# Kernel optimization log

Measured on AMD Instinct MI355X. Metric: run time of the kernel, lower is better.

Reference implementation:

```python
import jax, jax.numpy as jnp
import numpy as np

B, S, V, H, L, NH, DH, F, T = 256, 64, 21128, 768, 12, 12, 64, 3072, 11


def _layernorm(x, g, b):
    m = x.mean(-1, keepdims=True)
    v = ((x - m) ** 2).mean(-1, keepdims=True)
    return (x - m) / jnp.sqrt(v + 1e-12) * g + b


def setup_inputs():
    key = jax.random.key(0)
    ks = iter(jax.random.split(key, 24))
    std = 0.02
    w = lambda shape: jax.random.normal(next(ks), shape, jnp.float32) * std
    return {
        "input_ids": jax.random.randint(next(ks), (B, S), 0, V),
        "attention_mask": jnp.ones((B, S), jnp.int32),
        "label": jax.random.randint(next(ks), (B, S), 0, T),
        "word_emb": w((V, H)),
        "pos_emb": w((S, H)),
        "tok_emb": w((2, H)),
        "emb_ln_g": jnp.ones((H,), jnp.float32),
        "emb_ln_b": jnp.zeros((H,), jnp.float32),
        "Wqkv": w((L, H, 3 * H)),
        "bqkv": jnp.zeros((L, 3 * H), jnp.float32),
        "Wo": w((L, H, H)),
        "bo": jnp.zeros((L, H), jnp.float32),
        "ln1_g": jnp.ones((L, H), jnp.float32),
        "ln1_b": jnp.zeros((L, H), jnp.float32),
        "W1": w((L, H, F)),
        "b1": jnp.zeros((L, F), jnp.float32),
        "W2": w((L, F, H)),
        "b2": jnp.zeros((L, H), jnp.float32),
        "ln2_g": jnp.ones((L, H), jnp.float32),
        "ln2_b": jnp.zeros((L, H), jnp.float32),
        "fc_w": w((H, T)),
        "fc_b": jnp.zeros((T,), jnp.float32),
        "crf_start": w((T,)),
        "crf_end": w((T,)),
        "crf_trans": w((T, T)),
    }


def _encode(ids, mask, word_emb, pos_emb, tok_emb, eg, eb, layer_params):
    x = word_emb[ids] + pos_emb[None] + tok_emb[0][None, None]  # [B,S,H]
    x = _layernorm(x, eg, eb)
    bias = (1.0 - mask.astype(x.dtype))[:, None, None, :] * -1e9  # [B,1,1,S]

    def layer(x, p):
        Wqkv, bqkv, Wo, bo, g1, b1n, W1, b1, W2, b2, g2, b2n = p
        q, k, v = jnp.split(x @ Wqkv + bqkv, 3, axis=-1)
        sh = lambda t: t.reshape(B, S, NH, DH).transpose(0, 2, 1, 3)
        att = jax.nn.softmax(
            jnp.einsum("bhqd,bhkd->bhqk", sh(q), sh(k)) / jnp.sqrt(jnp.float32(DH)) + bias, -1
        )
        o = jnp.einsum("bhqk,bhkd->bhqd", att, sh(v)).transpose(0, 2, 1, 3).reshape(B, S, H)
        x = _layernorm(x + o @ Wo + bo, g1, b1n)
        h = jax.nn.gelu(x @ W1 + b1)
        x = _layernorm(x + h @ W2 + b2, g2, b2n)
        return x, None

    x, _ = jax.lax.scan(layer, x, layer_params)
    return x


def _crf_llh(em, tags, maskf, start, end, trans):
    # torchcrf log-likelihood, batch_first. em:[B,S,T] tags:[B,S] maskf:[B,S]
    bidx = jnp.arange(B)
    score = start[tags[:, 0]] + em[bidx, 0, tags[:, 0]]

    def num_step(s, xs):
        e_t, tp, tc, m = xs
        return s + (trans[tp, tc] + e_t[bidx, tc]) * m, None

    score, _ = jax.lax.scan(
        num_step, score,
        (em[:, 1:].transpose(1, 0, 2), tags[:, :-1].T, tags[:, 1:].T, maskf[:, 1:].T),
    )
    last_idx = maskf.sum(-1).astype(jnp.int32) - 1
    score = score + end[tags[bidx, last_idx]]

    alpha = start[None] + em[:, 0]  # [B,T]

    def den_step(a, xs):
        e_t, m = xs
        nxt = jax.scipy.special.logsumexp(a[:, :, None] + trans[None] + e_t[:, None, :], axis=1)
        return jnp.where(m[:, None] > 0, nxt, a), None

    alpha, _ = jax.lax.scan(den_step, alpha, (em[:, 1:].transpose(1, 0, 2), maskf[:, 1:].T))
    denom = jax.scipy.special.logsumexp(alpha + end[None], axis=1)
    return score - denom


def _viterbi(em, maskf, start, end, trans):
    bidx = jnp.arange(B)

    def step(s, xs):
        e_t, m = xs
        cand = s[:, :, None] + trans[None]  # [B,T_prev,T_cur]
        best_prev = jnp.argmax(cand, axis=1)  # [B,T]
        ns = jnp.max(cand, axis=1) + e_t
        return jnp.where(m[:, None] > 0, ns, s), best_prev

    score, hist = jax.lax.scan(
        step, start[None] + em[:, 0], (em[:, 1:].transpose(1, 0, 2), maskf[:, 1:].T)
    )  # hist: [S-1,B,T]
    last = jnp.argmax(score + end[None], axis=1)  # [B]

    def back(t, xs):
        h, m = xs
        nt = jnp.where(m > 0, h[bidx, t], t)
        return nt, nt

    _, prev_tags = jax.lax.scan(back, last, (hist, maskf[:, 1:].T), reverse=True)
    return jnp.concatenate([prev_tags.transpose(1, 0), last[:, None]], axis=1)  # [B,S]


def reference(input_ids, attention_mask, label, word_emb, pos_emb, tok_emb, emb_ln_g, emb_ln_b,
              Wqkv, bqkv, Wo, bo, ln1_g, ln1_b, W1, b1, W2, b2, ln2_g, ln2_b,
              fc_w, fc_b, crf_start, crf_end, crf_trans):
    lp = (Wqkv, bqkv, Wo, bo, ln1_g, ln1_b, W1, b1, W2, b2, ln2_g, ln2_b)
    x = _encode(input_ids, attention_mask, word_emb, pos_emb, tok_emb, emb_ln_g, emb_ln_b, lp)
    logits = x @ fc_w + fc_b  # [B,S,T]
    maskf = attention_mask.astype(jnp.float32)
    loss = -jnp.mean(_crf_llh(logits, label, maskf, crf_start, crf_end, crf_trans))
    pred = _viterbi(logits, maskf, crf_start, crf_end, crf_trans)
    return pred, loss
```

## Files before the change

kernel.cpp:

```cpp
#include <hip/hip_runtime.h>
#include <hip/hip_bf16.h>
#include <math.h>

namespace {

constexpr int B = 256, S = 64, H = 768, L = 12, NH = 12, F = 3072, T = 11;
constexpr int BS = B * S;
constexpr int RC = 8192;
constexpr int NCH = BS / RC;

typedef __attribute__((ext_vector_type(8))) short short8;
typedef __attribute__((ext_vector_type(4))) float f32x4;

__device__ __forceinline__ float gelu_tanh(float v) {
  float u = 0.7978845608028654f * (v + 0.044715f * v * v * v);
  u = fminf(fmaxf(u, -10.f), 10.f);
  float t = __expf(2.f * u);
  return 0.5f * v * (1.0f + (t - 1.f) / (t + 1.f));
}

__device__ __forceinline__ ushort f2bf(float v) {
  union { float f; unsigned u; } c; c.f = v;
  unsigned r = (c.u + 0x7fffu + ((c.u >> 16) & 1u)) >> 16;
  return (ushort)r;
}
__device__ __forceinline__ float bf2f(ushort u) {
  union { unsigned u; float f; } c; c.u = ((unsigned)u) << 16;
  return c.f;
}
__device__ __forceinline__ void split2(float v, ushort& hi, ushort& lo) {
  hi = f2bf(v);
  lo = f2bf(v - bf2f(hi));
}
__device__ __forceinline__ float join2(ushort hi, ushort lo) {
  return bf2f(hi) + bf2f(lo);
}
__device__ __forceinline__ int pcol(int c) { return ((c >> 5) << 6) + (c & 31); }

#define GLOAD_LDS16(gptr, ldsptr)                                                        \
  __builtin_amdgcn_global_load_lds((const __attribute__((address_space(1))) void*)(gptr), \
                                   (__attribute__((address_space(3))) void*)(ldsptr), 16, 0, 0)

template <int MODE>
__global__ __launch_bounds__(256, 2) void gemm_mfma(const ushort* __restrict__ A,
                                                    const ushort* __restrict__ Bw,
                                                    const float* __restrict__ bias,
                                                    float* __restrict__ outF,
                                                    ushort* __restrict__ outU,
                                                    int lda2, int ldb2, int ldc2,
                                                    int ldcF, int zStrideF, int ktiles) {
  __shared__ ushort sA[2][128 * 64];
  __shared__ ushort sB[2][128 * 64];
  const int tid = threadIdx.x;
  const int w = tid >> 6;
  const int lane = tid & 63;
  const int wm = w >> 1;
  const int wn = w & 1;

  const int gx = gridDim.x, gy = gridDim.y;
  const int flat = ((int)blockIdx.z * gy + blockIdx.y) * gx + blockIdx.x;
  const int q8 = (gx * gy * (int)gridDim.z) >> 3;
  const int swz = (flat & 7) * q8 + (flat >> 3);
  const int bx = swz % gx;
  const int by = (swz / gx) % gy;
  const int bz = swz / (gx * gy);
  const int bm = by * 128;
  const int bn = bx * 128;
  const int k0 = bz * ktiles * 64;

  const int srow = lane >> 3;
  const int sblk = (lane & 7) ^ srow;
  const ushort* Ab = A + (size_t)(bm + w * 32 + srow) * lda2 + k0 + sblk * 8;
  const ushort* Bb = Bw + (size_t)(bn + w * 32 + srow) * ldb2 + k0 + sblk * 8;

#define STAGE(buf, tk)                                                            \
  do {                                                                            \
    _Pragma("unroll") for (int i_ = 0; i_ < 4; ++i_) {                            \
      GLOAD_LDS16(Ab + (size_t)(tk) * 64 + (size_t)(i_ * 8) * lda2,               \
                  &sA[buf][(w * 32 + i_ * 8) * 64]);                              \
      GLOAD_LDS16(Bb + (size_t)(tk) * 64 + (size_t)(i_ * 8) * ldb2,               \
                  &sB[buf][(w * 32 + i_ * 8) * 64]);                              \
    }                                                                             \
  } while (0)

  const int fr = lane & 15;
  const int s7 = fr & 7;
  const int jb = lane >> 4;
  const int hOff = (jb ^ s7) << 3;
  const int lOff = ((4 + jb) ^ s7) << 3;

  f32x4 acc[4][4] = {};
  const int NT = ktiles;

  STAGE(0, 0);
  asm volatile("s_waitcnt vmcnt(0)" ::: "memory");
  __builtin_amdgcn_s_barrier();

  for (int t = 0; t < NT; ++t) {
    const int cur = t & 1;
    if (t + 1 < NT) STAGE(cur ^ 1, t + 1);

    short8 ah[4], al[4];
#pragma unroll
    for (int mi = 0; mi < 4; ++mi) {
      const ushort* baseA = &sA[cur][(wm * 64 + mi * 16 + fr) * 64];
      ah[mi] = *(const short8*)(baseA + hOff);
      al[mi] = *(const short8*)(baseA + lOff);
    }
#pragma unroll
    for (int ni = 0; ni < 4; ++ni) {
      const ushort* baseB = &sB[cur][(wn * 64 + ni * 16 + fr) * 64];
      short8 bh = *(const short8*)(baseB + hOff);
      short8 bl = *(const short8*)(baseB + lOff);
      __builtin_amdgcn_s_setprio(1);
#pragma unroll
      for (int mi = 0; mi < 4; ++mi) {
        acc[mi][ni] = __builtin_amdgcn_mfma_f32_16x16x32_bf16(ah[mi], bh, acc[mi][ni], 0, 0, 0);
        acc[mi][ni] = __builtin_amdgcn_mfma_f32_16x16x32_bf16(ah[mi], bl, acc[mi][ni], 0, 0, 0);
        acc[mi][ni] = __builtin_amdgcn_mfma_f32_16x16x32_bf16(al[mi], bh, acc[mi][ni], 0, 0, 0);
      }
      __builtin_amdgcn_s_setprio(0);
      if (ni == 3) asm volatile("s_waitcnt vmcnt(0)" ::: "memory");
      __builtin_amdgcn_s_barrier();
    }
  }
#undef STAGE

  const int erow = jb << 2;
#pragma unroll
  for (int ni = 0; ni < 4; ++ni) {
    const int col = bn + wn * 64 + ni * 16 + fr;
    const float bv = (MODE == 3) ? 0.f : bias[col];
    const int cb = pcol(col);
#pragma unroll
    for (int mi = 0; mi < 4; ++mi) {
#pragma unroll
      for (int e = 0; e < 4; ++e) {
        const int row = bm + wm * 64 + mi * 16 + erow + e;
        float v = acc[mi][ni][e] + bv;
        if (MODE == 1 || MODE == 2) {
          if (MODE == 1) v = gelu_tanh(v);
          ushort hi, lo;
          split2(v, hi, lo);
          outU[(size_t)row * ldc2 + cb] = hi;
          outU[(size_t)row * ldc2 + cb + 32] = lo;
        } else {
          outF[(size_t)bz * zStrideF + (size_t)row * ldcF + col] = v;
        }
      }
    }
  }
}

__global__ __launch_bounds__(256) void convert_w_t(const float* __restrict__ W,
                                                   ushort* __restrict__ WI, int K, int N) {
  __shared__ float tile[32][33];
  const int kb = blockIdx.y * 32, nb = blockIdx.x * 32;
  const int tr = threadIdx.x >> 5;
  const int tc = threadIdx.x & 31;
#pragma unroll
  for (int p = 0; p < 4; ++p) {
    int r = tr + p * 8;
    tile[r][tc] = W[(size_t)(kb + r) * N + nb + tc];
  }
  __syncthreads();
  const int kblk = kb >> 5;
#pragma unroll
  for (int p = 0; p < 4; ++p) {
    int n = tr + p * 8;
    float v = tile[tc][n];
    ushort hi, lo;
    split2(v, hi, lo);
    size_t o = (size_t)(nb + n) * (2 * K) + (size_t)kblk * 64 + tc;
    WI[o] = hi;
    WI[o + 32] = lo;
  }
}

__global__ __launch_bounds__(256) void attn_kernel(ushort* __restrict__ qkv,
                                                   const int* __restrict__ mask) {
  __shared__ float smem[64 * 64 + 64 * 66 + 64 * 64];
  float (*Qs)[64] = (float (*)[64])smem;
  float (*KsT)[66] = (float (*)[66])(smem + 64 * 64);
  float (*Vs)[64] = (float (*)[64])(smem + 64 * 64 + 64 * 66);
  float (*Ps)[65] = (float (*)[65])smem;

  const int bl = blockIdx.x / NH;
  const int hh = blockIdx.x % NH;
  const int tid = threadIdx.x;
  const int lane = tid & 63;
  const int w = tid >> 6;

  for (int i = 0; i < 16; ++i) {
    int idx = tid + i * 256;
    int r = idx >> 6, d = idx & 63;
    size_t rowb = (size_t)(bl * 64 + r) * 4608;
    int off = hh * 128 + pcol(d);
    Qs[r][d] = join2(qkv[rowb + off], qkv[rowb + off + 32]);
    KsT[d][r] = join2(qkv[rowb + 1536 + off], qkv[rowb + 1536 + off + 32]);
    Vs[r][d] = join2(qkv[rowb + 3072 + off], qkv[rowb + 3072 + off + 32]);
  }
  __syncthreads();

  float sc[16];
#pragma unroll
  for (int i = 0; i < 16; ++i) sc[i] = 0.f;
  for (int d = 0; d < 64; ++d) {
    float kv = KsT[d][lane];
#pragma unroll
    for (int i = 0; i < 16; ++i) sc[i] += Qs[w + 4 * i][d] * kv;
  }
  __syncthreads();
  float biask = (1.0f - (float)mask[bl * S + lane]) * -1e9f;
#pragma unroll
  for (int i = 0; i < 16; ++i) Ps[w + 4 * i][lane] = sc[i] * 0.125f + biask;
  __syncthreads();

  if (tid < 64) {
    int qr = tid;
    float mx = -1e30f;
    for (int k = 0; k < 64; ++k) mx = fmaxf(mx, Ps[qr][k]);
    float sum = 0.f;
    for (int k = 0; k < 64; ++k) {
      float e = expf(Ps[qr][k] - mx);
      Ps[qr][k] = e;
      sum += e;
    }
    float inv = 1.0f / sum;
    for (int k = 0; k < 64; ++k) Ps[qr][k] *= inv;
  }
  __syncthreads();

  float o[16];
#pragma unroll
  for (int i = 0; i < 16; ++i) o[i] = 0.f;
  for (int k = 0; k < 64; ++k) {
    float vv = Vs[k][lane];
#pragma unroll
    for (int i = 0; i < 16; ++i) o[i] += Ps[w + 4 * i][k] * vv;
  }
  const int ooff = hh * 128 + pcol(lane);
#pragma unroll
  for (int i = 0; i < 16; ++i) {
    int qr = w + 4 * i;
    size_t rowb = (size_t)(bl * 64 + qr) * 4608;
    ushort hi, lo;
    split2(o[i], hi, lo);
    qkv[rowb + ooff] = hi;
    qkv[rowb + ooff + 32] = lo;
  }
}

__global__ __launch_bounds__(256) void embed_ln_kernel(const int* __restrict__ ids,
                                                       const float* __restrict__ we,
                                                       const float* __restrict__ pe,
                                                       const float* __restrict__ te,
                                                       const float* __restrict__ g,
                                                       const float* __restrict__ bta,
                                                       ushort* __restrict__ xhl) {
  __shared__ float buf[H];
  __shared__ float red[256];
  const int row = blockIdx.x;
  const int s = row % S;
  const int tid = threadIdx.x;
  const int id = ids[row];
  float local = 0.f;
  for (int i = tid; i < H; i += 256) {
    float v = we[(size_t)id * H + i] + pe[(size_t)s * H + i] + te[i];
    buf[i] = v;
    local += v;
  }
  red[tid] = local;
  __syncthreads();
  for (int st = 128; st > 0; st >>= 1) {
    if (tid < st) red[tid] += red[tid + st];
    __syncthreads();
  }
  float mean = red[0] * (1.0f / H);
  __syncthreads();
  float ls = 0.f;
  for (int i = tid; i < H; i += 256) {
    float d = buf[i] - mean;
    ls += d * d;
  }
  red[tid] = ls;
  __syncthreads();
  for (int st = 128; st > 0; st >>= 1) {
    if (tid < st) red[tid] += red[tid + st];
    __syncthreads();
  }
  float inv = 1.0f / sqrtf(red[0] * (1.0f / H) + 1e-12f);
  for (int i = tid; i < H; i += 256) {
    float o = (buf[i] - mean) * inv * g[i] + bta[i];
    int cb = pcol(i);
    ushort hi, lo;
    split2(o, hi, lo);
    xhl[(size_t)row * (2 * H) + cb] = hi;
    xhl[(size_t)row * (2 * H) + cb + 32] = lo;
  }
}

__global__ __launch_bounds__(256) void add_ln_kernel(ushort* __restrict__ xhl,
                                                     const float* __restrict__ pz0,
                                                     const float* __restrict__ pz1,
                                                     int prs,
                                                     const float* __restrict__ biasv,
                                                     const float* __restrict__ g,
                                                     const float* __restrict__ bta) {
  __shared__ float buf[H];
  __shared__ float red[256];
  const size_t row = blockIdx.x;
  const int tid = threadIdx.x;
  float local = 0.f;
  for (int i = tid; i < H; i += 256) {
    int cb = pcol(i);
    float v = join2(xhl[row * (2 * H) + cb], xhl[row * (2 * H) + cb + 32]) +
              ((pz0[row * (size_t)prs + i] + pz1[row * (size_t)prs + i]) + biasv[i]);
    buf[i] = v;
    local += v;
  }
  red[tid] = local;
  __syncthreads();
  for (int st = 128; st > 0; st >>= 1) {
    if (tid < st) red[tid] += red[tid + st];
    __syncthreads();
  }
  float mean = red[0] * (1.0f / H);
  __syncthreads();
  float ls = 0.f;
  for (int i = tid; i < H; i += 256) {
    float d = buf[i] - mean;
    ls += d * d;
  }
  red[tid] = ls;
  __syncthreads();
  for (int st = 128; st > 0; st >>= 1) {
    if (tid < st) red[tid] += red[tid + st];
    __syncthreads();
  }
  float inv = 1.0f / sqrtf(red[0] * (1.0f / H) + 1e-12f);
  for (int i = tid; i < H; i += 256) {
    float o = (buf[i] - mean) * inv * g[i] + bta[i];
    int cb = pcol(i);
    ushort hi, lo;
    split2(o, hi, lo);
    xhl[row * (2 * H) + cb] = hi;
    xhl[row * (2 * H) + cb + 32] = lo;
  }
}

__global__ __launch_bounds__(256) void fc_kernel(const ushort* __restrict__ xhl,
                                                 const float* __restrict__ w,
                                                 const float* __restrict__ bias,
                                                 float* __restrict__ logits) {
  __shared__ float xs[H];
  const size_t row = blockIdx.x;
  const int tid = threadIdx.x;
  for (int i = tid; i < H; i += 256) {
    int cb = pcol(i);
    xs[i] = join2(xhl[row * (2 * H) + cb], xhl[row * (2 * H) + cb + 32]);
  }
  __syncthreads();
  const int j = tid >> 4, l = tid & 15;
  if (j < T) {
    float s = 0.f;
    for (int k = l; k < H; k += 16) s += xs[k] * w[(size_t)k * T + j];
#pragma unroll
    for (int d = 8; d > 0; d >>= 1) s += __shfl_down(s, d, 16);
    if (l == 0) logits[row * T + j] = s + bias[j];
  }
}

__global__ __launch_bounds__(64) void crf_llh_kernel(const float* __restrict__ em,
                                                     const int* __restrict__ label,
                                                     const int* __restrict__ mask,
                                                     const float* __restrict__ start,
                                                     const float* __restrict__ endw,
                                                     const float* __restrict__ trans,
                                                     float* __restrict__ llh) {
  const int b = blockIdx.x;
  const int c = threadIdx.x;
  __shared__ float alpha[T];
  __shared__ float tr[T][T];
  for (int i = c; i < T * T; i += 64) tr[i / T][i % T] = trans[i];
  if (c < T) alpha[c] = start[c] + em[(size_t)b * S * T + c];
  __syncthreads();
  for (int s = 1; s < S; ++s) {
    float a = 0.f;
    if (c < T) {
      float mx = -1e30f;
      for (int p = 0; p < T; ++p) mx = fmaxf(mx, alpha[p] + tr[p][c]);
      float sum = 0.f;
      for (int p = 0; p < T; ++p) sum += expf(alpha[p] + tr[p][c] - mx);
      a = mx + logf(sum) + em[((size_t)b * S + s) * T + c];
    }
    __syncthreads();
    if (c < T) {
      float m = (float)mask[b * S + s];
      alpha[c] = (m > 0.f) ? a : alpha[c];
    }
    __syncthreads();
  }
  if (c == 0) {
    float mx = -1e30f;
    for (int p = 0; p < T; ++p) mx = fmaxf(mx, alpha[p] + endw[p]);
    float sum = 0.f;
    for (int p = 0; p < T; ++p) sum += expf(alpha[p] + endw[p] - mx);
    float denom = mx + logf(sum);

    int t0 = label[b * S];
    float score = start[t0] + em[(size_t)b * S * T + t0];
    int prev = t0;
    for (int s = 1; s < S; ++s) {
      int tc = label[b * S + s];
      float m = (float)mask[b * S + s];
      score += (tr[prev][tc] + em[((size_t)b * S + s) * T + tc]) * m;
      prev = tc;
    }
    int msum = 0;
    for (int s = 0; s < S; ++s) msum += mask[b * S + s];
    score += endw[label[b * S + (msum - 1)]];
    llh[b] = score - denom;
  }
}

__global__ __launch_bounds__(256) void loss_kernel(const float* __restrict__ llh,
                                                   float* __restrict__ out) {
  __shared__ float red[256];
  const int tid = threadIdx.x;
  red[tid] = llh[tid];
  __syncthreads();
  for (int st = 128; st > 0; st >>= 1) {
    if (tid < st) red[tid] += red[tid + st];
    __syncthreads();
  }
  if (tid == 0) out[BS] = -red[0] * (1.0f / B);
}

__global__ __launch_bounds__(64) void viterbi_kernel(const float* __restrict__ em,
                                                     const int* __restrict__ mask,
                                                     const float* __restrict__ start,
                                                     const float* __restrict__ endw,
                                                     const float* __restrict__ trans,
                                                     float* __restrict__ pred) {
  const int b = blockIdx.x;
  const int c = threadIdx.x;
  __shared__ float sc[T];
  __shared__ float tr[T][T];
  __shared__ int hist[S - 1][T];
  for (int i = c; i < T * T; i += 64) tr[i / T][i % T] = trans[i];
  if (c < T) sc[c] = start[c] + em[(size_t)b * S * T + c];
  __syncthreads();
  for (int s = 1; s < S; ++s) {
    float bestv = -1e30f;
    int bestp = 0;
    if (c < T) {
      for (int p = 0; p < T; ++p) {
        float v = sc[p] + tr[p][c];
        if (v > bestv) { bestv = v; bestp = p; }
      }
      hist[s - 1][c] = bestp;
    }
    __syncthreads();
    if (c < T) {
      float m = (float)mask[b * S + s];
      sc[c] = (m > 0.f) ? (bestv + em[((size_t)b * S + s) * T + c]) : sc[c];
    }
    __syncthreads();
  }
  if (c == 0) {
    float bv = -1e30f;
    int last = 0;
    for (int p = 0; p < T; ++p) {
      float v = sc[p] + endw[p];
      if (v > bv) { bv = v; last = p; }
    }
    pred[b * S + (S - 1)] = (float)last;
    int t = last;
    for (int hs = S - 2; hs >= 0; --hs) {
      if (mask[b * S + hs + 1] > 0) t = hist[hs][t];
      pred[b * S + hs] = (float)t;
    }
  }
}

}

extern "C" void kernel_launch(void* const* d_in, const int* in_sizes, int n_in,
                              void* d_out, int out_size, void* d_ws, size_t ws_size,
                              hipStream_t stream) {
  (void)in_sizes; (void)n_in; (void)out_size; (void)ws_size;
  const int* input_ids = (const int*)d_in[0];
  const int* attn_mask = (const int*)d_in[1];
  const int* label = (const int*)d_in[2];
  const float* word_emb = (const float*)d_in[3];
  const float* pos_emb = (const float*)d_in[4];
  const float* tok_emb = (const float*)d_in[5];
  const float* eg = (const float*)d_in[6];
  const float* ebt = (const float*)d_in[7];
  const float* Wqkv = (const float*)d_in[8];
  const float* bqkv = (const float*)d_in[9];
  const float* Wo = (const float*)d_in[10];
  const float* bo = (const float*)d_in[11];
  const float* ln1g = (const float*)d_in[12];
  const float* ln1b = (const float*)d_in[13];
  const float* W1 = (const float*)d_in[14];
  const float* b1 = (const float*)d_in[15];
  const float* W2 = (const float*)d_in[16];
  const float* b2 = (const float*)d_in[17];
  const float* ln2g = (const float*)d_in[18];
  const float* ln2b = (const float*)d_in[19];
  const float* fc_w = (const float*)d_in[20];
  const float* fc_b = (const float*)d_in[21];
  const float* crf_start = (const float*)d_in[22];
  const float* crf_end = (const float*)d_in[23];
  const float* crf_trans = (const float*)d_in[24];
  float* out = (float*)d_out;

  char* p = (char*)d_ws;
  ushort* xhl = (ushort*)p;    p += (size_t)BS * 2 * H * 2;
  ushort* wQ = (ushort*)p;     p += (size_t)3 * H * 2 * H * 2;
  ushort* wO = (ushort*)p;     p += (size_t)H * 2 * H * 2;
  ushort* wF1 = (ushort*)p;    p += (size_t)F * 2 * H * 2;
  ushort* wF2 = (ushort*)p;    p += (size_t)H * 2 * F * 2;
  char* big = p;               p += (size_t)BS * 3 * H * 4;
  float* logits = (float*)p;   p += (size_t)BS * T * 4;
  float* llh = (float*)p;      p += (size_t)B * 4;
  ushort* qkvP = (ushort*)big;
  float* qf = (float*)big;
  ushort* hU = (ushort*)big;
  float* pf = (float*)(big + (size_t)RC * F * 4);

  embed_ln_kernel<<<BS, 256, 0, stream>>>(input_ids, word_emb, pos_emb, tok_emb, eg, ebt, xhl);

  for (int l = 0; l < L; ++l) {
    const float* wqkv_l = Wqkv + (size_t)l * H * 3 * H;
    const float* bqkv_l = bqkv + (size_t)l * 3 * H;
    const float* wo_l = Wo + (size_t)l * H * H;
    const float* bo_l = bo + (size_t)l * H;
    const float* g1 = ln1g + (size_t)l * H;
    const float* be1 = ln1b + (size_t)l * H;
    const float* w1_l = W1 + (size_t)l * H * F;
    const float* b1_l = b1 + (size_t)l * F;
    const float* w2_l = W2 + (size_t)l * F * H;
    const float* b2_l = b2 + (size_t)l * H;
    const float* g2 = ln2g + (size_t)l * H;
    const float* be2 = ln2b + (size_t)l * H;

    convert_w_t<<<dim3(3 * H / 32, H / 32), 256, 0, stream>>>(wqkv_l, wQ, H, 3 * H);
    convert_w_t<<<dim3(H / 32, H / 32), 256, 0, stream>>>(wo_l, wO, H, H);
    convert_w_t<<<dim3(F / 32, H / 32), 256, 0, stream>>>(w1_l, wF1, H, F);
    convert_w_t<<<dim3(H / 32, F / 32), 256, 0, stream>>>(w2_l, wF2, F, H);

    gemm_mfma<2><<<dim3(3 * H / 128, BS / 128, 1), 256, 0, stream>>>(
        xhl, wQ, bqkv_l, nullptr, qkvP, 2 * H, 2 * H, 2 * 3 * H, 0, 0, H / 32);
    attn_kernel<<<B * NH, 256, 0, stream>>>(qkvP, attn_mask);
    gemm_mfma<3><<<dim3(H / 128, BS / 128, 2), 256, 0, stream>>>(
        qkvP, wO, nullptr, qf + H, nullptr, 2 * 3 * H, 2 * H, 0, 3 * H, H, H / 64);
    add_ln_kernel<<<BS, 256, 0, stream>>>(xhl, qf + H, qf + 2 * H, 3 * H, bo_l, g1, be1);

    for (int ch = 0; ch < NCH; ++ch) {
      gemm_mfma<1><<<dim3(F / 128, RC / 128, 1), 256, 0, stream>>>(
          xhl + (size_t)ch * RC * 2 * H, wF1, b1_l, nullptr, hU, 2 * H, 2 * H, 2 * F,
          0, 0, H / 32);
      gemm_mfma<3><<<dim3(H / 128, RC / 128, 2), 256, 0, stream>>>(
          hU, wF2, nullptr, pf, nullptr, 2 * F, 2 * F, 0, H, RC * H, F / 64);
      add_ln_kernel<<<RC, 256, 0, stream>>>(xhl + (size_t)ch * RC * 2 * H, pf,
                                            pf + (size_t)RC * H, H, b2_l, g2, be2);
    }
  }

  fc_kernel<<<BS, 256, 0, stream>>>(xhl, fc_w, fc_b, logits);
  crf_llh_kernel<<<B, 64, 0, stream>>>(logits, label, attn_mask, crf_start, crf_end, crf_trans, llh);
  loss_kernel<<<1, 256, 0, stream>>>(llh, out);
  viterbi_kernel<<<B, 64, 0, stream>>>(logits, attn_mask, crf_start, crf_end, crf_trans, out);
}
```

Before: 11.27 ms.

## Use 512-thread GEMM with wider N tiles and triple-buffered LDS pipeline

The split-bf16 MFMA GEMM moves from 256-thread 128x128 tiles with double buffering to 512-thread blocks whose N tile is templated (128x256 or 128x128), fed by a three-stage LDS ring with two tiles prefetched ahead. Waits use partial vmcnt counts, so global loads overlap compute across iterations rather than draining at every step. This is meant to hide global-to-LDS latency and raise MFMA utilisation. In exchange it uses more LDS per block, which caps occupancy at one block per CU, and the last two iterations issue throwaway loads of tile 0.

```diff
diff --git a/kernel.cpp b/kernel.cpp
--- a/kernel.cpp
+++ b/kernel.cpp
@@ -41,21 +41,22 @@
   __builtin_amdgcn_global_load_lds((const __attribute__((address_space(1))) void*)(gptr), \
                                    (__attribute__((address_space(3))) void*)(ldsptr), 16, 0, 0)
 
-template <int MODE>
-__global__ __launch_bounds__(256, 2) void gemm_mfma(const ushort* __restrict__ A,
+template <int MODE, int NIQ>
+__global__ __launch_bounds__(512, 1) void gemm_mfma(const ushort* __restrict__ A,
                                                     const ushort* __restrict__ Bw,
                                                     const float* __restrict__ bias,
                                                     float* __restrict__ outF,
                                                     ushort* __restrict__ outU,
                                                     int lda2, int ldb2, int ldc2,
                                                     int ldcF, int zStrideF, int ktiles) {
-  __shared__ ushort sA[2][128 * 64];
-  __shared__ ushort sB[2][128 * 64];
+  constexpr int BN = 64 * NIQ;
+  __shared__ ushort sA[3][128 * 64];
+  __shared__ ushort sB[3][BN * 64];
   const int tid = threadIdx.x;
   const int w = tid >> 6;
   const int lane = tid & 63;
-  const int wm = w >> 1;
-  const int wn = w & 1;
+  const int wm = w >> 2;
+  const int wn = w & 3;
 
   const int gx = gridDim.x, gy = gridDim.y;
   const int flat = ((int)blockIdx.z * gy + blockIdx.y) * gx + blockIdx.x;
@@ -65,22 +66,23 @@
   const int by = (swz / gx) % gy;
   const int bz = swz / (gx * gy);
   const int bm = by * 128;
-  const int bn = bx * 128;
+  const int bn = bx * BN;
   const int k0 = bz * ktiles * 64;
 
   const int srow = lane >> 3;
   const int sblk = (lane & 7) ^ srow;
-  const ushort* Ab = A + (size_t)(bm + w * 32 + srow) * lda2 + k0 + sblk * 8;
-  const ushort* Bb = Bw + (size_t)(bn + w * 32 + srow) * ldb2 + k0 + sblk * 8;
-
-#define STAGE(buf, tk)                                                            \
-  do {                                                                            \
-    _Pragma("unroll") for (int i_ = 0; i_ < 4; ++i_) {                            \
-      GLOAD_LDS16(Ab + (size_t)(tk) * 64 + (size_t)(i_ * 8) * lda2,               \
-                  &sA[buf][(w * 32 + i_ * 8) * 64]);                              \
-      GLOAD_LDS16(Bb + (size_t)(tk) * 64 + (size_t)(i_ * 8) * ldb2,               \
-                  &sB[buf][(w * 32 + i_ * 8) * 64]);                              \
-    }                                                                             \
+  const ushort* Ab0 = A + (size_t)(bm + 16 * w + srow) * lda2 + k0 + sblk * 8;
+  const ushort* Bb0 = Bw + (size_t)(bn + 8 * NIQ * w + srow) * ldb2 + k0 + sblk * 8;
+
+#define STAGE(buf, tk)                                                           \
+  do {                                                                           \
+    GLOAD_LDS16(Ab0 + (size_t)(tk) * 64, &sA[buf][(16 * w) * 64]);               \
+    GLOAD_LDS16(Ab0 + (size_t)(tk) * 64 + (size_t)8 * lda2,                      \
+                &sA[buf][(16 * w + 8) * 64]);                                    \
+    _Pragma("unroll") for (int j_ = 0; j_ < NIQ; ++j_) {                         \
+      GLOAD_LDS16(Bb0 + (size_t)(tk) * 64 + (size_t)(8 * j_) * ldb2,             \
+                  &sB[buf][(8 * NIQ * w + 8 * j_) * 64]);                        \
+    }                                                                            \
   } while (0)
 
   const int fr = lane & 15;
@@ -89,27 +91,30 @@
   const int hOff = (jb ^ s7) << 3;
   const int lOff = ((4 + jb) ^ s7) << 3;
 
-  f32x4 acc[4][4] = {};
+  f32x4 acc[4][NIQ] = {};
   const int NT = ktiles;
 
   STAGE(0, 0);
-  asm volatile("s_waitcnt vmcnt(0)" ::: "memory");
-  __builtin_amdgcn_s_barrier();
+  STAGE(1, 1);
+  int c0 = 0, c1 = 1, c2 = 2;
 
   for (int t = 0; t < NT; ++t) {
-    const int cur = t & 1;
-    if (t + 1 < NT) STAGE(cur ^ 1, t + 1);
+    const int tk = (t + 2 < NT) ? (t + 2) : 0;
+    STAGE(c2, tk);
+    if constexpr (NIQ == 4) asm volatile("s_waitcnt vmcnt(12)" ::: "memory");
+    else                    asm volatile("s_waitcnt vmcnt(8)" ::: "memory");
+    __builtin_amdgcn_s_barrier();
 
     short8 ah[4], al[4];
 #pragma unroll
     for (int mi = 0; mi < 4; ++mi) {
-      const ushort* baseA = &sA[cur][(wm * 64 + mi * 16 + fr) * 64];
+      const ushort* baseA = &sA[c0][(wm * 64 + mi * 16 + fr) * 64];
       ah[mi] = *(const short8*)(baseA + hOff);
       al[mi] = *(const short8*)(baseA + lOff);
     }
 #pragma unroll
-    for (int ni = 0; ni < 4; ++ni) {
-      const ushort* baseB = &sB[cur][(wn * 64 + ni * 16 + fr) * 64];
+    for (int ni = 0; ni < NIQ; ++ni) {
+      const ushort* baseB = &sB[c0][(wn * 16 * NIQ + ni * 16 + fr) * 64];
       short8 bh = *(const short8*)(baseB + hOff);
       short8 bl = *(const short8*)(baseB + lOff);
       __builtin_amdgcn_s_setprio(1);
@@ -120,16 +125,19 @@
         acc[mi][ni] = __builtin_amdgcn_mfma_f32_16x16x32_bf16(al[mi], bh, acc[mi][ni], 0, 0, 0);
       }
       __builtin_amdgcn_s_setprio(0);
-      if (ni == 3) asm volatile("s_waitcnt vmcnt(0)" ::: "memory");
-      __builtin_amdgcn_s_barrier();
-    }
+      if (ni + 1 < NIQ) __builtin_amdgcn_s_barrier();
+    }
+    asm volatile("s_waitcnt lgkmcnt(0)" ::: "memory");
+    __builtin_amdgcn_s_barrier();
+    const int tmp = c0; c0 = c1; c1 = c2; c2 = tmp;
   }
 #undef STAGE
+  asm volatile("s_waitcnt vmcnt(0)" ::: "memory");
 
   const int erow = jb << 2;
 #pragma unroll
-  for (int ni = 0; ni < 4; ++ni) {
-    const int col = bn + wn * 64 + ni * 16 + fr;
+  for (int ni = 0; ni < NIQ; ++ni) {
+    const int col = bn + wn * 16 * NIQ + ni * 16 + fr;
     const float bv = (MODE == 3) ? 0.f : bias[col];
     const int cb = pcol(col);
 #pragma unroll
@@ -552,18 +560,18 @@
     convert_w_t<<<dim3(F / 32, H / 32), 256, 0, stream>>>(w1_l, wF1, H, F);
     convert_w_t<<<dim3(H / 32, F / 32), 256, 0, stream>>>(w2_l, wF2, F, H);
 
-    gemm_mfma<2><<<dim3(3 * H / 128, BS / 128, 1), 256, 0, stream>>>(
+    gemm_mfma<2, 4><<<dim3(3 * H / 256, BS / 128, 1), 512, 0, stream>>>(
         xhl, wQ, bqkv_l, nullptr, qkvP, 2 * H, 2 * H, 2 * 3 * H, 0, 0, H / 32);
     attn_kernel<<<B * NH, 256, 0, stream>>>(qkvP, attn_mask);
-    gemm_mfma<3><<<dim3(H / 128, BS / 128, 2), 256, 0, stream>>>(
+    gemm_mfma<3, 4><<<dim3(H / 256, BS / 128, 2), 512, 0, stream>>>(
         qkvP, wO, nullptr, qf + H, nullptr, 2 * 3 * H, 2 * H, 0, 3 * H, H, H / 64);
     add_ln_kernel<<<BS, 256, 0, stream>>>(xhl, qf + H, qf + 2 * H, 3 * H, bo_l, g1, be1);
 
     for (int ch = 0; ch < NCH; ++ch) {
-      gemm_mfma<1><<<dim3(F / 128, RC / 128, 1), 256, 0, stream>>>(
+      gemm_mfma<1, 4><<<dim3(F / 256, RC / 128, 1), 512, 0, stream>>>(
           xhl + (size_t)ch * RC * 2 * H, wF1, b1_l, nullptr, hU, 2 * H, 2 * H, 2 * F,
           0, 0, H / 32);
-      gemm_mfma<3><<<dim3(H / 128, RC / 128, 2), 256, 0, stream>>>(
+      gemm_mfma<3, 2><<<dim3(H / 128, RC / 128, 2), 512, 0, stream>>>(
           hU, wF2, nullptr, pf, nullptr, 2 * F, 2 * F, 0, H, RC * H, F / 64);
       add_ln_kernel<<<RC, 256, 0, stream>>>(xhl + (size_t)ch * RC * 2 * H, pf,
                                             pf + (size_t)RC * H, H, b2_l, g2, be2);
```

After: 13.38 ms. 18.8% more time.

## Use 256-row 8-wave GEMM tiles with interleaved staged prefetch

Applied to the files above, without the earlier changes.

Replaces the 128x128 4-wave MFMA GEMM with a 512-thread kernel using 256-row tiles and 256- or 128-column tiles, so each loaded operand feeds more MFMAs. Next-tile global-to-LDS loads are split into chunks and interleaved with the four compute phases of each k-step, with finer barriers, instead of one bulk prefetch. The aim is higher arithmetic intensity and better overlap of loads with MFMA work. In exchange the kernel uses more registers and LDS and launches fewer, larger blocks, which may cost occupancy and leave the last wave of blocks partly empty.

```diff
diff --git a/kernel.cpp b/kernel.cpp
--- a/kernel.cpp
+++ b/kernel.cpp
@@ -41,21 +41,22 @@
   __builtin_amdgcn_global_load_lds((const __attribute__((address_space(1))) void*)(gptr), \
                                    (__attribute__((address_space(3))) void*)(ldsptr), 16, 0, 0)
 
-template <int MODE>
-__global__ __launch_bounds__(256, 2) void gemm_mfma(const ushort* __restrict__ A,
-                                                    const ushort* __restrict__ Bw,
-                                                    const float* __restrict__ bias,
-                                                    float* __restrict__ outF,
-                                                    ushort* __restrict__ outU,
-                                                    int lda2, int ldb2, int ldc2,
-                                                    int ldcF, int zStrideF, int ktiles) {
-  __shared__ ushort sA[2][128 * 64];
-  __shared__ ushort sB[2][128 * 64];
+template <int MODE, int NI>
+__global__ __launch_bounds__(512, 2) void gemm8p(const ushort* __restrict__ A,
+                                                 const ushort* __restrict__ Bw,
+                                                 const float* __restrict__ bias,
+                                                 float* __restrict__ outF,
+                                                 ushort* __restrict__ outU,
+                                                 int lda2, int ldb2, int ldc2,
+                                                 int ldcF, int zStrideF, int ktiles) {
+  constexpr int BN = 64 * NI;
+  __shared__ ushort sA[2][256 * 64];
+  __shared__ ushort sB[2][BN * 64];
   const int tid = threadIdx.x;
   const int w = tid >> 6;
   const int lane = tid & 63;
-  const int wm = w >> 1;
-  const int wn = w & 1;
+  const int wm = w >> 2;
+  const int wn = w & 3;
 
   const int gx = gridDim.x, gy = gridDim.y;
   const int flat = ((int)blockIdx.z * gy + blockIdx.y) * gx + blockIdx.x;
@@ -64,24 +65,21 @@
   const int bx = swz % gx;
   const int by = (swz / gx) % gy;
   const int bz = swz / (gx * gy);
-  const int bm = by * 128;
-  const int bn = bx * 128;
+  const int bm = by * 256;
+  const int bn = bx * BN;
   const int k0 = bz * ktiles * 64;
 
   const int srow = lane >> 3;
   const int sblk = (lane & 7) ^ srow;
-  const ushort* Ab = A + (size_t)(bm + w * 32 + srow) * lda2 + k0 + sblk * 8;
-  const ushort* Bb = Bw + (size_t)(bn + w * 32 + srow) * ldb2 + k0 + sblk * 8;
-
-#define STAGE(buf, tk)                                                            \
-  do {                                                                            \
-    _Pragma("unroll") for (int i_ = 0; i_ < 4; ++i_) {                            \
-      GLOAD_LDS16(Ab + (size_t)(tk) * 64 + (size_t)(i_ * 8) * lda2,               \
-                  &sA[buf][(w * 32 + i_ * 8) * 64]);                              \
-      GLOAD_LDS16(Bb + (size_t)(tk) * 64 + (size_t)(i_ * 8) * ldb2,               \
-                  &sB[buf][(w * 32 + i_ * 8) * 64]);                              \
-    }                                                                             \
-  } while (0)
+  const ushort* Ab0 = A + (size_t)(bm + 32 * w + srow) * lda2 + k0 + sblk * 8;
+  const ushort* Bb0 = Bw + (size_t)(bn + (BN / 8) * w + srow) * ldb2 + k0 + sblk * 8;
+
+#define STAGE_A(buf, tk, c)                                                     \
+  GLOAD_LDS16(Ab0 + (size_t)(tk) * 64 + (size_t)(8 * (c)) * lda2,               \
+              &sA[buf][(32 * w + 8 * (c)) * 64])
+#define STAGE_B(buf, tk, c)                                                     \
+  GLOAD_LDS16(Bb0 + (size_t)(tk) * 64 + (size_t)(8 * (c)) * ldb2,               \
+              &sB[buf][((BN / 8) * w + 8 * (c)) * 64])
 
   const int fr = lane & 15;
   const int s7 = fr & 7;
@@ -89,54 +87,108 @@
   const int hOff = (jb ^ s7) << 3;
   const int lOff = ((4 + jb) ^ s7) << 3;
 
-  f32x4 acc[4][4] = {};
+  f32x4 acc[8][NI] = {};
   const int NT = ktiles;
 
-  STAGE(0, 0);
-  asm volatile("s_waitcnt vmcnt(0)" ::: "memory");
-  __builtin_amdgcn_s_barrier();
+  {
+#pragma unroll
+    for (int c = 0; c < NI; ++c) STAGE_B(0, 0, c);
+#pragma unroll
+    for (int c = 0; c < 4; ++c) STAGE_A(0, 0, c);
+    asm volatile("s_waitcnt vmcnt(0)" ::: "memory");
+    __builtin_amdgcn_s_barrier();
+  }
 
   for (int t = 0; t < NT; ++t) {
-    const int cur = t & 1;
-    if (t + 1 < NT) STAGE(cur ^ 1, t + 1);
-
-    short8 ah[4], al[4];
-#pragma unroll
-    for (int mi = 0; mi < 4; ++mi) {
-      const ushort* baseA = &sA[cur][(wm * 64 + mi * 16 + fr) * 64];
-      ah[mi] = *(const short8*)(baseA + hOff);
-      al[mi] = *(const short8*)(baseA + lOff);
-    }
-#pragma unroll
-    for (int ni = 0; ni < 4; ++ni) {
-      const ushort* baseB = &sB[cur][(wn * 64 + ni * 16 + fr) * 64];
-      short8 bh = *(const short8*)(baseB + hOff);
-      short8 bl = *(const short8*)(baseB + lOff);
+    const int cur = t & 1, nxt = cur ^ 1;
+    const int tk = (t + 1 < NT) ? (t + 1) : 0;
+
+    STAGE_B(nxt, tk, 0);
+    if constexpr (NI == 4) {
+      STAGE_B(nxt, tk, 1);
+      asm volatile("s_waitcnt vmcnt(2)" ::: "memory");
+    } else {
+      asm volatile("s_waitcnt vmcnt(1)" ::: "memory");
+    }
+    __builtin_amdgcn_s_barrier();
+    __builtin_amdgcn_sched_barrier(0);
+
+    short8 bh[NI], bl[NI];
+#pragma unroll
+    for (int ni = 0; ni < NI; ++ni) {
+      const ushort* baseB = &sB[cur][(wn * (BN / 4) + ni * 16 + fr) * 64];
+      bh[ni] = *(const short8*)(baseB + hOff);
+      bl[ni] = *(const short8*)(baseB + lOff);
+    }
+    {
+      short8 ah[2], al[2];
+#pragma unroll
+      for (int j = 0; j < 2; ++j) {
+        const ushort* baseA = &sA[cur][(wm * 128 + j * 16 + fr) * 64];
+        ah[j] = *(const short8*)(baseA + hOff);
+        al[j] = *(const short8*)(baseA + lOff);
+      }
       __builtin_amdgcn_s_setprio(1);
 #pragma unroll
-      for (int mi = 0; mi < 4; ++mi) {
-        acc[mi][ni] = __builtin_amdgcn_mfma_f32_16x16x32_bf16(ah[mi], bh, acc[mi][ni], 0, 0, 0);
-        acc[mi][ni] = __builtin_amdgcn_mfma_f32_16x16x32_bf16(ah[mi], bl, acc[mi][ni], 0, 0, 0);
-        acc[mi][ni] = __builtin_amdgcn_mfma_f32_16x16x32_bf16(al[mi], bh, acc[mi][ni], 0, 0, 0);
+      for (int j = 0; j < 2; ++j)
+#pragma unroll
+        for (int ni = 0; ni < NI; ++ni) {
+          acc[j][ni] = __builtin_amdgcn_mfma_f32_16x16x32_bf16(ah[j], bh[ni], acc[j][ni], 0, 0, 0);
+          acc[j][ni] = __builtin_amdgcn_mfma_f32_16x16x32_bf16(ah[j], bl[ni], acc[j][ni], 0, 0, 0);
+          acc[j][ni] = __builtin_amdgcn_mfma_f32_16x16x32_bf16(al[j], bh[ni], acc[j][ni], 0, 0, 0);
+        }
+      __builtin_amdgcn_s_setprio(0);
+    }
+    __builtin_amdgcn_s_barrier();
+
+#pragma unroll
+    for (int q = 1; q < 4; ++q) {
+      short8 ah[2], al[2];
+#pragma unroll
+      for (int j = 0; j < 2; ++j) {
+        const ushort* baseA = &sA[cur][(wm * 128 + (2 * q + j) * 16 + fr) * 64];
+        ah[j] = *(const short8*)(baseA + hOff);
+        al[j] = *(const short8*)(baseA + lOff);
+      }
+      if (q == 1) {
+        if constexpr (NI == 4) { STAGE_B(nxt, tk, 2); STAGE_B(nxt, tk, 3); }
+        else                   { STAGE_B(nxt, tk, 1); }
+      } else if (q == 2) {
+        STAGE_A(nxt, tk, 0); STAGE_A(nxt, tk, 1);
+      } else {
+        STAGE_A(nxt, tk, 2); STAGE_A(nxt, tk, 3);
+      }
+      __builtin_amdgcn_s_barrier();
+      __builtin_amdgcn_s_setprio(1);
+#pragma unroll
+      for (int j = 0; j < 2; ++j) {
+        const int mi = 2 * q + j;
+#pragma unroll
+        for (int ni = 0; ni < NI; ++ni) {
+          acc[mi][ni] = __builtin_amdgcn_mfma_f32_16x16x32_bf16(ah[j], bh[ni], acc[mi][ni], 0, 0, 0);
+          acc[mi][ni] = __builtin_amdgcn_mfma_f32_16x16x32_bf16(ah[j], bl[ni], acc[mi][ni], 0, 0, 0);
+          acc[mi][ni] = __builtin_amdgcn_mfma_f32_16x16x32_bf16(al[j], bh[ni], acc[mi][ni], 0, 0, 0);
+        }
       }
       __builtin_amdgcn_s_setprio(0);
-      if (ni == 3) asm volatile("s_waitcnt vmcnt(0)" ::: "memory");
       __builtin_amdgcn_s_barrier();
     }
   }
-#undef STAGE
+#undef STAGE_A
+#undef STAGE_B
+  asm volatile("s_waitcnt vmcnt(0)" ::: "memory");
 
   const int erow = jb << 2;
 #pragma unroll
-  for (int ni = 0; ni < 4; ++ni) {
-    const int col = bn + wn * 64 + ni * 16 + fr;
+  for (int ni = 0; ni < NI; ++ni) {
+    const int col = bn + wn * (BN / 4) + ni * 16 + fr;
     const float bv = (MODE == 3) ? 0.f : bias[col];
     const int cb = pcol(col);
 #pragma unroll
-    for (int mi = 0; mi < 4; ++mi) {
+    for (int mi = 0; mi < 8; ++mi) {
 #pragma unroll
       for (int e = 0; e < 4; ++e) {
-        const int row = bm + wm * 64 + mi * 16 + erow + e;
+        const int row = bm + wm * 128 + mi * 16 + erow + e;
         float v = acc[mi][ni][e] + bv;
         if (MODE == 1 || MODE == 2) {
           if (MODE == 1) v = gelu_tanh(v);
@@ -552,18 +604,18 @@
     convert_w_t<<<dim3(F / 32, H / 32), 256, 0, stream>>>(w1_l, wF1, H, F);
     convert_w_t<<<dim3(H / 32, F / 32), 256, 0, stream>>>(w2_l, wF2, F, H);
 
-    gemm_mfma<2><<<dim3(3 * H / 128, BS / 128, 1), 256, 0, stream>>>(
+    gemm8p<2, 4><<<dim3(3 * H / 256, BS / 256, 1), 512, 0, stream>>>(
         xhl, wQ, bqkv_l, nullptr, qkvP, 2 * H, 2 * H, 2 * 3 * H, 0, 0, H / 32);
     attn_kernel<<<B * NH, 256, 0, stream>>>(qkvP, attn_mask);
-    gemm_mfma<3><<<dim3(H / 128, BS / 128, 2), 256, 0, stream>>>(
+    gemm8p<3, 4><<<dim3(H / 256, BS / 256, 2), 512, 0, stream>>>(
         qkvP, wO, nullptr, qf + H, nullptr, 2 * 3 * H, 2 * H, 0, 3 * H, H, H / 64);
     add_ln_kernel<<<BS, 256, 0, stream>>>(xhl, qf + H, qf + 2 * H, 3 * H, bo_l, g1, be1);
 
     for (int ch = 0; ch < NCH; ++ch) {
-      gemm_mfma<1><<<dim3(F / 128, RC / 128, 1), 256, 0, stream>>>(
+      gemm8p<1, 4><<<dim3(F / 256, RC / 256, 1), 512, 0, stream>>>(
           xhl + (size_t)ch * RC * 2 * H, wF1, b1_l, nullptr, hU, 2 * H, 2 * H, 2 * F,
           0, 0, H / 32);
-      gemm_mfma<3><<<dim3(H / 128, RC / 128, 2), 256, 0, stream>>>(
+      gemm8p<3, 2><<<dim3(H / 128, RC / 256, 2), 512, 0, stream>>>(
           hU, wF2, nullptr, pf, nullptr, 2 * F, 2 * F, 0, H, RC * H, F / 64);
       add_ln_kernel<<<RC, 256, 0, stream>>>(xhl + (size_t)ch * RC * 2 * H, pf,
                                             pf + (size_t)RC * H, H, b2_l, g2, be2);
```

After: 13.77 ms. 22.2% more time.

## Drop LDS double buffering in GEMM to raise occupancy to four blocks

Applied to the files above, without the earlier changes.

The GEMM kernel moves from a double-buffered LDS pipeline, where the next tile is prefetched while the current one is computed, to a single buffer that loads, syncs, computes and syncs again on each k-tile. Launch bounds are raised from 2 to 4 blocks per CU, so other resident blocks are expected to hide load latency instead of in-block prefetch. All B fragments are now loaded up front and the MFMA loop is reordered. This adds an extra barrier per tile, removes intra-block overlap of loads and compute, and may cause register spills under the tighter register budget.

```diff
diff --git a/kernel.cpp b/kernel.cpp
--- a/kernel.cpp
+++ b/kernel.cpp
@@ -42,15 +42,15 @@
                                    (__attribute__((address_space(3))) void*)(ldsptr), 16, 0, 0)
 
 template <int MODE>
-__global__ __launch_bounds__(256, 2) void gemm_mfma(const ushort* __restrict__ A,
+__global__ __launch_bounds__(256, 4) void gemm_mfma(const ushort* __restrict__ A,
                                                     const ushort* __restrict__ Bw,
                                                     const float* __restrict__ bias,
                                                     float* __restrict__ outF,
                                                     ushort* __restrict__ outU,
                                                     int lda2, int ldb2, int ldc2,
                                                     int ldcF, int zStrideF, int ktiles) {
-  __shared__ ushort sA[2][128 * 64];
-  __shared__ ushort sB[2][128 * 64];
+  __shared__ ushort sA[128 * 64];
+  __shared__ ushort sB[128 * 64];
   const int tid = threadIdx.x;
   const int w = tid >> 6;
   const int lane = tid & 63;
@@ -73,16 +73,6 @@
   const ushort* Ab = A + (size_t)(bm + w * 32 + srow) * lda2 + k0 + sblk * 8;
   const ushort* Bb = Bw + (size_t)(bn + w * 32 + srow) * ldb2 + k0 + sblk * 8;
 
-#define STAGE(buf, tk)                                                            \
-  do {                                                                            \
-    _Pragma("unroll") for (int i_ = 0; i_ < 4; ++i_) {                            \
-      GLOAD_LDS16(Ab + (size_t)(tk) * 64 + (size_t)(i_ * 8) * lda2,               \
-                  &sA[buf][(w * 32 + i_ * 8) * 64]);                              \
-      GLOAD_LDS16(Bb + (size_t)(tk) * 64 + (size_t)(i_ * 8) * ldb2,               \
-                  &sB[buf][(w * 32 + i_ * 8) * 64]);                              \
-    }                                                                             \
-  } while (0)
-
   const int fr = lane & 15;
   const int s7 = fr & 7;
   const int jb = lane >> 4;
@@ -92,39 +82,39 @@
   f32x4 acc[4][4] = {};
   const int NT = ktiles;
 
-  STAGE(0, 0);
-  asm volatile("s_waitcnt vmcnt(0)" ::: "memory");
-  __builtin_amdgcn_s_barrier();
-
   for (int t = 0; t < NT; ++t) {
-    const int cur = t & 1;
-    if (t + 1 < NT) STAGE(cur ^ 1, t + 1);
-
-    short8 ah[4], al[4];
+#pragma unroll
+    for (int c = 0; c < 4; ++c) {
+      GLOAD_LDS16(Ab + (size_t)t * 64 + (size_t)(c * 8) * lda2, &sA[(w * 32 + c * 8) * 64]);
+      GLOAD_LDS16(Bb + (size_t)t * 64 + (size_t)(c * 8) * ldb2, &sB[(w * 32 + c * 8) * 64]);
+    }
+    __syncthreads();
+
+    short8 ah[4], al[4], bh[4], bl[4];
 #pragma unroll
     for (int mi = 0; mi < 4; ++mi) {
-      const ushort* baseA = &sA[cur][(wm * 64 + mi * 16 + fr) * 64];
+      const ushort* baseA = &sA[(wm * 64 + mi * 16 + fr) * 64];
       ah[mi] = *(const short8*)(baseA + hOff);
       al[mi] = *(const short8*)(baseA + lOff);
     }
 #pragma unroll
     for (int ni = 0; ni < 4; ++ni) {
-      const ushort* baseB = &sB[cur][(wn * 64 + ni * 16 + fr) * 64];
-      short8 bh = *(const short8*)(baseB + hOff);
-      short8 bl = *(const short8*)(baseB + lOff);
-      __builtin_amdgcn_s_setprio(1);
-#pragma unroll
-      for (int mi = 0; mi < 4; ++mi) {
-        acc[mi][ni] = __builtin_amdgcn_mfma_f32_16x16x32_bf16(ah[mi], bh, acc[mi][ni], 0, 0, 0);
-        acc[mi][ni] = __builtin_amdgcn_mfma_f32_16x16x32_bf16(ah[mi], bl, acc[mi][ni], 0, 0, 0);
-        acc[mi][ni] = __builtin_amdgcn_mfma_f32_16x16x32_bf16(al[mi], bh, acc[mi][ni], 0, 0, 0);
+      const ushort* baseB = &sB[(wn * 64 + ni * 16 + fr) * 64];
+      bh[ni] = *(const short8*)(baseB + hOff);
+      bl[ni] = *(const short8*)(baseB + lOff);
+    }
+    __builtin_amdgcn_s_setprio(1);
+#pragma unroll
+    for (int mi = 0; mi < 4; ++mi)
+#pragma unroll
+      for (int ni = 0; ni < 4; ++ni) {
+        acc[mi][ni] = __builtin_amdgcn_mfma_f32_16x16x32_bf16(ah[mi], bh[ni], acc[mi][ni], 0, 0, 0);
+        acc[mi][ni] = __builtin_amdgcn_mfma_f32_16x16x32_bf16(ah[mi], bl[ni], acc[mi][ni], 0, 0, 0);
+        acc[mi][ni] = __builtin_amdgcn_mfma_f32_16x16x32_bf16(al[mi], bh[ni], acc[mi][ni], 0, 0, 0);
       }
-      __builtin_amdgcn_s_setprio(0);
-      if (ni == 3) asm volatile("s_waitcnt vmcnt(0)" ::: "memory");
-      __builtin_amdgcn_s_barrier();
-    }
-  }
-#undef STAGE
+    __builtin_amdgcn_s_setprio(0);
+    __syncthreads();
+  }
 
   const int erow = jb << 2;
 #pragma unroll
```

Result: slower. 27.43 ms (+143.4%).
